# Kernel optimization log

Measured on AMD Instinct MI355X. Metric: run time of the kernel, lower is better.

## Reference

```python
import jax, jax.numpy as jnp
import numpy as np
from jax import lax


def conv2d_same(x, w):
    # x: [N,C,H,W], w: [O,I,3,3] -> [N,O,H,W], stride 1, padding 1
    return lax.conv_general_dilated(x, w, (1, 1), 'SAME',
                                    dimension_numbers=('NCHW', 'OIHW', 'NCHW'))


def bilinear_gather(x, py, px):
    # x: [N,C,H,W]; py,px: [N,K,H,W] float sampling coords (zero pad outside)
    # returns [N,C,K,H,W]
    N, C, H, W = x.shape
    y0f = jnp.floor(py)
    x0f = jnp.floor(px)
    wy = (py - y0f)[:, None]  # [N,1,K,H,W]
    wx = (px - x0f)[:, None]
    y0 = y0f.astype(jnp.int32)
    x0 = x0f.astype(jnp.int32)
    flat = x.reshape(N, C, H * W)

    def gather(yi, xi):
        valid = ((yi >= 0) & (yi < H) & (xi >= 0) & (xi < W))
        yc = jnp.clip(yi, 0, H - 1)
        xc = jnp.clip(xi, 0, W - 1)
        idx = (yc * W + xc).reshape(N, 1, -1)          # [N,1,K*H*W]
        g = jnp.take_along_axis(flat, jnp.broadcast_to(idx, (N, C, idx.shape[-1])), axis=2)
        g = g.reshape(N, C, *yi.shape[1:])             # [N,C,K,H,W]
        return g * valid.astype(x.dtype)[:, None]

    v00 = gather(y0, x0)
    v01 = gather(y0, x0 + 1)
    v10 = gather(y0 + 1, x0)
    v11 = gather(y0 + 1, x0 + 1)
    return (v00 * (1 - wy) * (1 - wx) + v01 * (1 - wy) * wx
            + v10 * wy * (1 - wx) + v11 * wy * wx)


def deform_conv(x, off, w, b):
    # x: [N,C,H,W]; off: [N,18,H,W] (dy,dx per 3x3 tap); w: [O,C,3,3]; b: [O]
    N, C, H, W = x.shape
    K = 9
    off = off.reshape(N, K, 2, H, W)
    kdy, kdx = jnp.meshgrid(jnp.arange(3) - 1, jnp.arange(3) - 1, indexing='ij')
    kdy = kdy.reshape(K).astype(x.dtype)
    kdx = kdx.reshape(K).astype(x.dtype)
    hh = jnp.arange(H, dtype=x.dtype)
    ww = jnp.arange(W, dtype=x.dtype)
    py = off[:, :, 0] + hh[None, None, :, None] + kdy[None, :, None, None]  # [N,K,H,W]
    px = off[:, :, 1] + ww[None, None, None, :] + kdx[None, :, None, None]
    sampled = bilinear_gather(x, py, px)               # [N,C,K,H,W]
    out = jnp.einsum('nckhw,ock->nohw', sampled, w.reshape(w.shape[0], C, K))
    return out + b[None, :, None, None]


def setup_inputs() -> dict:
    key = jax.random.key(0)
    ks = jax.random.split(key, 8)
    B, obj, C, H, W = 2, 4, 256, 48, 48
    return {
        'query': jax.random.normal(ks[0], (B, C, H, W), jnp.float32),
        'key': jax.random.normal(ks[1], (B, C, H, W), jnp.float32),
        'value': jax.random.normal(ks[2], (B, obj, C, H, W), jnp.float32),
        'off_conv_w': jax.random.normal(ks[3], (C, 2 * C, 3, 3), jnp.float32) * 0.02,
        'off_conv_b': jnp.zeros((C,), jnp.float32),
        'offp_w': jax.random.normal(ks[4], (18, C, 3, 3), jnp.float32) * 0.02,
        'offp_b': jnp.zeros((18,), jnp.float32),
        'deform_w': jax.random.normal(ks[5], (C, C, 3, 3), jnp.float32) * 0.02,
        'deform_b': jnp.zeros((C,), jnp.float32),
    }


def reference(query, key, value, off_conv_w, off_conv_b, offp_w, offp_b, deform_w, deform_b):
    B, obj, C, H, W = value.shape
    N = B * obj
    concat = jnp.concatenate([query, key], axis=1)                    # [B,2C,H,W]
    feat = conv2d_same(concat, off_conv_w) + off_conv_b[None, :, None, None]
    feat = jnp.broadcast_to(feat[:, None], (B, obj, C, H, W)).reshape(N, C, H, W)
    x = value.reshape(N, C, H, W)
    off = conv2d_same(feat, offp_w) + offp_b[None, :, None, None]     # [N,18,H,W]
    out = deform_conv(x, off, deform_w, deform_b)                     # [N,C,H,W]
    out = out.reshape(N, C, H * W).transpose(2, 0, 1)                 # [HW,N,C]
    q = jnp.broadcast_to(query[:, None], (B, obj, C, H, W)).reshape(N, C, H * W)
    return q.transpose(2, 0, 1) + out
```

## Files before the change

### kernel.cpp

```cpp
#include <hip/hip_runtime.h>

#define HH 48
#define WW 48
#define HWP 2304
#define CC 256
#define NB 8
#define QKROW 2305

typedef __attribute__((ext_vector_type(8))) short short8;
typedef __attribute__((ext_vector_type(4))) short bf16x4;
typedef __attribute__((ext_vector_type(4))) float floatx4;

static __device__ __forceinline__ unsigned short f2bf(float f) {
    union { float f; unsigned u; } v; v.f = f;
    unsigned r = v.u + 0x7fffu + ((v.u >> 16) & 1u);
    return (unsigned short)(r >> 16);
}
static __device__ __forceinline__ float bf2f(short v) {
    union { unsigned u; float f; } x; x.u = ((unsigned)(unsigned short)v) << 16;
    return x.f;
}

__global__ __launch_bounds__(256) void k_tr_qk(const float* __restrict__ q,
        const float* __restrict__ kk, unsigned short* __restrict__ qkT) {
    __shared__ float T[64][65];
    const int pg = blockIdx.x, cg = blockIdx.y;
    const int b = blockIdx.z >> 1, src = blockIdx.z & 1;
    const float* s = (src ? kk : q) + (size_t)b * CC * HWP;
    const int tx = threadIdx.x & 63, ty = threadIdx.x >> 6;
#pragma unroll
    for (int i = 0; i < 16; i++) {
        int cl = ty * 16 + i;
        T[cl][tx] = s[(size_t)(cg * 64 + cl) * HWP + pg * 64 + tx];
    }
    __syncthreads();
#pragma unroll
    for (int i = 0; i < 16; i++) {
        int pxl = ty * 16 + i;
        qkT[((size_t)b * QKROW + pg * 64 + pxl) * 512 + src * 256 + cg * 64 + tx]
            = f2bf(T[tx][pxl]);
    }
}

__global__ __launch_bounds__(256) void k_tr_v(const float* __restrict__ v,
                                              unsigned short* __restrict__ vT) {
    __shared__ float T[64][65];
    const int pg = blockIdx.x, cg = blockIdx.y, n = blockIdx.z;
    const float* s = v + (size_t)n * CC * HWP;
    const int tx = threadIdx.x & 63, ty = threadIdx.x >> 6;
#pragma unroll
    for (int i = 0; i < 16; i++) {
        int cl = ty * 16 + i;
        T[cl][tx] = s[(size_t)(cg * 64 + cl) * HWP + pg * 64 + tx];
    }
    __syncthreads();
#pragma unroll
    for (int i = 0; i < 16; i++) {
        int pxl = ty * 16 + i;
        vT[((size_t)n * HWP + pg * 64 + pxl) * 256 + cg * 64 + tx] = f2bf(T[tx][pxl]);
    }
}

__global__ __launch_bounds__(256) void k_prep_w(const float* __restrict__ w1,
        const float* __restrict__ dw, const float* __restrict__ w2,
        unsigned short* __restrict__ w1r, unsigned short* __restrict__ wdr,
        unsigned short* __restrict__ w2r, unsigned short* __restrict__ qkT,
        unsigned short* __restrict__ featb) {
    if (blockIdx.x == 7200) {
        int t = threadIdx.x;
#pragma unroll
        for (int b = 0; b < 2; b++) {
            qkT[((size_t)b * QKROW + HWP) * 512 + t] = 0;
            qkT[((size_t)b * QKROW + HWP) * 512 + 256 + t] = 0;
            featb[((size_t)b * QKROW + HWP) * 256 + t] = 0;
        }
        return;
    }
    int idx = blockIdx.x * 256 + threadIdx.x;
    if (idx < 1179648) {
        int j = idx & 7, l = (idx >> 3) & 63, mtg = (idx >> 9) & 15;
        int kk = (idx >> 13) & 15, tap = idx >> 17;
        int o = mtg * 16 + (l & 15);
        int c2 = kk * 32 + (l >> 4) * 8 + j;
        w1r[idx] = f2bf(w1[((size_t)o * 512 + c2) * 9 + tap]);
    } else if (idx < 1179648 + 589824) {
        int i2 = idx - 1179648;
        int j = i2 & 7, l = (i2 >> 3) & 63, mtg = (i2 >> 9) & 15;
        int kk = (i2 >> 13) & 7, tap = i2 >> 16;
        int o = mtg * 16 + (l & 15);
        int c = kk * 32 + (l >> 4) * 8 + j;
        wdr[i2] = f2bf(dw[((size_t)o * 256 + c) * 9 + tap]);
    } else {
        int i2 = idx - 1179648 - 589824;
        int j = i2 & 7, l = (i2 >> 3) & 63, mt = (i2 >> 9) & 1;
        int kk = (i2 >> 10) & 7, tap = i2 >> 13;
        int o = mt * 16 + (l & 15);
        int c = kk * 32 + (l >> 4) * 8 + j;
        w2r[i2] = (o < 18) ? f2bf(w2[((size_t)o * 256 + c) * 9 + tap]) : 0;
    }
}

__global__ __launch_bounds__(512, 4) void k_conv1(const unsigned short* __restrict__ qkT,
        const unsigned short* __restrict__ w1r, const float* __restrict__ b1,
        unsigned short* __restrict__ featb) {
    __shared__ __align__(16) unsigned short Bl[2][32 * 64 * 8];

    const int tid = threadIdx.x;
    const int pt = blockIdx.x;
    const int b  = blockIdx.y;
    const int oh = blockIdx.z;
    const int px0 = pt * 32;
    const int lane = tid & 63, wv = tid >> 6;
    const int lo = lane & 15, quad = lane >> 4;
    const int mtg = oh * 8 + wv;

    floatx4 acc[2];
    acc[0] = (floatx4)0.f; acc[1] = (floatx4)0.f;

    short8 R[4];
    auto stage_load = [&](int tap) {
        const int dy = tap / 3 - 1, dx = tap % 3 - 1;
#pragma unroll
        for (int k = 0; k < 4; k++) {
            int seg = tid + k * 512;
            int cl  = seg >> 6;
            int sl  = seg & 63;
            int px  = px0 + cl;
            int h = px / WW, w = px - (px / WW) * WW;
            bool val = (h + dy >= 0) && (h + dy < HH)
                       && (w + dx >= 0) && (w + dx < WW);
            int row = val ? (px + dy * WW + dx) : HWP;
            R[k] = *(const short8*)(qkT + ((size_t)b * QKROW + row) * 512 + sl * 8);
        }
    };

    stage_load(0);
    int buf = 0;

    for (int tap = 0; tap < 9; tap++) {
        unsigned short* sb = &Bl[buf][0];
#pragma unroll
        for (int k = 0; k < 4; k++) {
            int seg = tid + k * 512;
            int cl = seg >> 6, sl = seg & 63;
            int slw = sl ^ (cl & 7);
            *(short8*)(sb + ((size_t)cl * 64 + slw) * 8) = R[k];
        }
        __syncthreads();

        if (tap < 8) stage_load(tap + 1);

        const unsigned short* afr = w1r + (((size_t)tap * 16 * 16 + mtg) * 64 + lane) * 8;
#pragma unroll 4
        for (int ks = 0; ks < 16; ks++) {
            short8 a = *(const short8*)(afr + (size_t)ks * 16 * 512);
#pragma unroll
            for (int nt = 0; nt < 2; nt++) {
                int cl = nt * 16 + lo;
                int slot = (ks * 4 + quad) ^ (cl & 7);
                short8 bf = *(const short8*)(sb + ((size_t)cl * 64 + slot) * 8);
                acc[nt] = __builtin_amdgcn_mfma_f32_16x16x32_bf16(a, bf, acc[nt], 0, 0, 0);
            }
        }
        buf ^= 1;
    }

    const int o = mtg * 16 + quad * 4;
    const float b0 = b1[o], bb1 = b1[o + 1], bb2 = b1[o + 2], bb3 = b1[o + 3];
#pragma unroll
    for (int nt = 0; nt < 2; nt++) {
        int px = px0 + nt * 16 + lo;
        bf16x4 pk;
        pk[0] = (short)f2bf(acc[nt][0] + b0);
        pk[1] = (short)f2bf(acc[nt][1] + bb1);
        pk[2] = (short)f2bf(acc[nt][2] + bb2);
        pk[3] = (short)f2bf(acc[nt][3] + bb3);
        *(bf16x4*)(featb + ((size_t)b * QKROW + px) * 256 + o) = pk;
    }
}

__global__ __launch_bounds__(256) void k_conv2(const unsigned short* __restrict__ featb,
        const unsigned short* __restrict__ w2r, float* __restrict__ off9) {
    const int tid = threadIdx.x;
    const int pb = blockIdx.x;
    const int b  = blockIdx.y;
    const int tap = blockIdx.z;
    const int lane = tid & 63, wv = tid >> 6;
    const int lo = lane & 15, quad = lane >> 4;
    const int pp = pb * 64 + wv * 16 + lo;
    const int h = pp / WW, w = pp - (pp / WW) * WW;
    const int dy = tap / 3 - 1, dx = tap % 3 - 1;
    const bool val = (h + dy >= 0) && (h + dy < HH) && (w + dx >= 0) && (w + dx < WW);
    const int row = val ? (pp + dy * WW + dx) : HWP;

    const unsigned short* brow = featb + ((size_t)b * QKROW + row) * 256 + quad * 8;
    const unsigned short* afr = w2r + (((size_t)tap * 8 * 2) * 64 + lane) * 8;

    floatx4 acc[2];
    acc[0] = (floatx4)0.f; acc[1] = (floatx4)0.f;
#pragma unroll
    for (int ks = 0; ks < 8; ks++) {
        short8 bf = *(const short8*)(brow + ks * 32);
        const unsigned short* ak = afr + (size_t)ks * 2 * 512;
        short8 a0 = *(const short8*)(ak);
        short8 a1 = *(const short8*)(ak + 512);
        acc[0] = __builtin_amdgcn_mfma_f32_16x16x32_bf16(a0, bf, acc[0], 0, 0, 0);
        acc[1] = __builtin_amdgcn_mfma_f32_16x16x32_bf16(a1, bf, acc[1], 0, 0, 0);
    }

    float* dst = off9 + (((size_t)tap * 2 + b) * HWP + pp) * 32;
#pragma unroll
    for (int mt = 0; mt < 2; mt++) {
        int o = mt * 16 + quad * 4;
        *(floatx4*)(dst + o) = acc[mt];
    }
}

__global__ __launch_bounds__(256) void k_osum(const float* __restrict__ off9,
        const float* __restrict__ b2, float* __restrict__ off) {
    int i = blockIdx.x * 256 + threadIdx.x;
    int b = i / (18 * HWP);
    int r = i - b * 18 * HWP;
    int o = r / HWP, px = r - o * HWP;
    float s = b2[o];
#pragma unroll
    for (int t = 0; t < 9; t++)
        s += off9[(((size_t)t * 2 + b) * HWP + px) * 32 + o];
    off[i] = s;
}

__global__ __launch_bounds__(512, 2) void k_deform(const unsigned short* __restrict__ vT,
        const float* __restrict__ off, const unsigned short* __restrict__ wdr,
        const float* __restrict__ db, const float* __restrict__ q,
        float* __restrict__ out) {
    __shared__ __align__(16) unsigned short Sl[2][80 * 256];

    const int tid = threadIdx.x;
    const int bid = blockIdx.x;
    const int c0 = (((bid & 7) << 5) + (bid >> 3)) * 72;
    const int lane = tid & 63, wv = tid >> 6;
    const int lo = lane & 15, quad = lane >> 4;
    const int colg = tid >> 5;
    const int slice = tid & 31;

    int u_pq[5];
    float u_m[5];
    const float* u_off[5];
    const unsigned short* u_vT[5];
#pragma unroll
    for (int u = 0; u < 5; u++) {
        int cl = colg + u * 16;
        int cg = min(c0 + cl, 18431);
        int pq = cg >> 3, n = cg & 7;
        u_pq[u] = pq;
        u_m[u]  = (cl < 72) ? 1.f : 0.f;
        u_off[u] = off + (size_t)(n >> 2) * 18 * HWP + pq;
        u_vT[u]  = vT + (size_t)n * HWP * 256 + slice * 8;
    }

    floatx4 acc[2][5];
#pragma unroll
    for (int mt = 0; mt < 2; mt++)
#pragma unroll
        for (int nt = 0; nt < 5; nt++) acc[mt][nt] = (floatx4)0.f;

    short8 P[5][4];
    float  cwt[5][4];
    float  ndy[5], ndx[5];

    auto prefetch_off = [&](int tap) {
#pragma unroll
        for (int u = 0; u < 5; u++) {
            ndy[u] = u_off[u][(2 * tap) * HWP];
            ndx[u] = u_off[u][(2 * tap + 1) * HWP];
        }
    };

    auto prefetch_body = [&](int tap) {
        const float kdy = (float)(tap / 3 - 1), kdx = (float)(tap % 3 - 1);
#pragma unroll
        for (int u = 0; u < 5; u++) {
            int pq = u_pq[u];
            int h = pq / WW, w = pq - (pq / WW) * WW;
            float py = ndy[u] + (float)h + kdy;
            float px = ndx[u] + (float)w + kdx;
            float y0f = floorf(py), x0f = floorf(px);
            int y0 = (int)y0f, x0 = (int)x0f;
            float fy = py - y0f, fx = px - x0f;
            bool y0ok = (y0 >= 0) & (y0 < HH), y1ok = (y0 >= -1) & (y0 < HH - 1);
            bool x0ok = (x0 >= 0) & (x0 < WW), x1ok = (x0 >= -1) & (x0 < WW - 1);
            int y0c = min(max(y0, 0), HH - 1), y1c = min(max(y0 + 1, 0), HH - 1);
            int x0c = min(max(x0, 0), WW - 1), x1c = min(max(x0 + 1, 0), WW - 1);
            const unsigned short* r0 = u_vT[u] + (size_t)(y0c * WW + x0c) * 256;
            const unsigned short* r1 = u_vT[u] + (size_t)(y0c * WW + x1c) * 256;
            const unsigned short* r2 = u_vT[u] + (size_t)(y1c * WW + x0c) * 256;
            const unsigned short* r3 = u_vT[u] + (size_t)(y1c * WW + x1c) * 256;
            float m = u_m[u];
            cwt[u][0] = (y0ok && x0ok) ? m * (1.f - fy) * (1.f - fx) : 0.f;
            cwt[u][1] = (y0ok && x1ok) ? m * (1.f - fy) * fx         : 0.f;
            cwt[u][2] = (y1ok && x0ok) ? m * fy * (1.f - fx)         : 0.f;
            cwt[u][3] = (y1ok && x1ok) ? m * fy * fx                 : 0.f;
            P[u][0] = *(const short8*)(r0);
            P[u][1] = *(const short8*)(r1);
            P[u][2] = *(const short8*)(r2);
            P[u][3] = *(const short8*)(r3);
        }
    };

    prefetch_off(0);
    prefetch_body(0);
    int buf = 0;

    for (int tap = 0; tap < 9; tap++) {
        if (tap < 8) prefetch_off(tap + 1);
        unsigned short* sb = &Sl[buf][0];
#pragma unroll
        for (int u = 0; u < 5; u++) {
            float w0 = cwt[u][0], w1 = cwt[u][1], w2 = cwt[u][2], w3 = cwt[u][3];
            short8 ov;
#pragma unroll
            for (int j = 0; j < 8; j++) {
                float s = w0 * bf2f(P[u][0][j]) + w1 * bf2f(P[u][1][j])
                        + w2 * bf2f(P[u][2][j]) + w3 * bf2f(P[u][3][j]);
                ov[j] = (short)f2bf(s);
            }
            int cl = colg + u * 16;
            int slot = slice ^ (cl & 7);
            *(short8*)(sb + cl * 256 + slot * 8) = ov;
        }
        __syncthreads();

        if (tap < 8) prefetch_body(tap + 1);

        const unsigned short* afr = wdr + (((size_t)tap * 8 * 16 + wv * 2) * 64 + lane) * 8;
#pragma unroll
        for (int ks = 0; ks < 8; ks++) {
            const unsigned short* ak = afr + (size_t)ks * 16 * 512;
            short8 a0 = *(const short8*)(ak);
            short8 a1 = *(const short8*)(ak + 512);
#pragma unroll
            for (int nt = 0; nt < 5; nt++) {
                int cl = nt * 16 + lo;
                int slot = (ks * 4 + quad) ^ (cl & 7);
                short8 bf = *(const short8*)(sb + cl * 256 + slot * 8);
                acc[0][nt] = __builtin_amdgcn_mfma_f32_16x16x32_bf16(a0, bf, acc[0][nt], 0, 0, 0);
                acc[1][nt] = __builtin_amdgcn_mfma_f32_16x16x32_bf16(a1, bf, acc[1][nt], 0, 0, 0);
            }
        }
        __syncthreads();
        buf ^= 1;
    }

#pragma unroll
    for (int mt = 0; mt < 2; mt++) {
        int o = wv * 32 + mt * 16 + quad * 4;
        float d0 = db[o], d1 = db[o + 1], d2 = db[o + 2], d3 = db[o + 3];
#pragma unroll
        for (int nt = 0; nt < 5; nt++) {
            int cl = nt * 16 + lo;
            if (cl < 72) {
                int cg = c0 + cl;
                int pq = cg >> 3, b = (cg & 7) >> 2;
                floatx4 r = acc[mt][nt];
                r[0] += d0 + q[((size_t)b * CC + o + 0) * HWP + pq];
                r[1] += d1 + q[((size_t)b * CC + o + 1) * HWP + pq];
                r[2] += d2 + q[((size_t)b * CC + o + 2) * HWP + pq];
                r[3] += d3 + q[((size_t)b * CC + o + 3) * HWP + pq];
                *(floatx4*)(out + (size_t)cg * CC + o) = r;
            }
        }
    }
}

extern "C" void kernel_launch(void* const* d_in, const int* in_sizes, int n_in,
                              void* d_out, int out_size, void* d_ws, size_t ws_size,
                              hipStream_t stream) {
    const float* q  = (const float*)d_in[0];
    const float* k  = (const float*)d_in[1];
    const float* v  = (const float*)d_in[2];
    const float* w1 = (const float*)d_in[3];
    const float* b1 = (const float*)d_in[4];
    const float* w2 = (const float*)d_in[5];
    const float* b2 = (const float*)d_in[6];
    const float* dw = (const float*)d_in[7];
    const float* db = (const float*)d_in[8];
    float* out = (float*)d_out;

    float* off   = (float*)d_ws;
    float* feat3 = off + 82944;
    float* off9  = feat3 + 3538944;
    unsigned short* qkT   = (unsigned short*)(off9 + 1327104);
    unsigned short* vT    = qkT + 2360320;
    unsigned short* featb = vT + 4718592;
    unsigned short* w1r   = featb + 1180160;
    unsigned short* wdr   = w1r + 1179648;
    unsigned short* w2r   = wdr + 589824;

    hipLaunchKernelGGL(k_tr_qk, dim3(36, 4, 4),  dim3(256), 0, stream, q, k, qkT);
    hipLaunchKernelGGL(k_tr_v,  dim3(36, 4, 8),  dim3(256), 0, stream, v, vT);
    hipLaunchKernelGGL(k_prep_w,dim3(7201),      dim3(256), 0, stream, w1, dw, w2, w1r, wdr, w2r, qkT, featb);
    hipLaunchKernelGGL(k_conv1, dim3(72, 2, 2),  dim3(512), 0, stream, qkT, w1r, b1, featb);
    hipLaunchKernelGGL(k_conv2, dim3(36, 2, 9),  dim3(256), 0, stream, featb, w2r, off9);
    hipLaunchKernelGGL(k_osum,  dim3(324),       dim3(256), 0, stream, off9, b2, off);
    hipLaunchKernelGGL(k_deform,dim3(256),       dim3(512), 0, stream, vT, off, wdr, db, q, out);
}
```

Measured before the change: 208.5 us.

## Merge transpose kernels and add pixel-major query copy for deform epilogue

Folds the q/k and v transpose kernels into one launch indexed by blockIdx.z. While transposing the query, it also writes an fp32 pixel-major copy of it. The deform epilogue then reads the residual query as one contiguous float4 instead of four strided scalar loads spaced HWP apart. This costs an extra fp32 write of the query in the transpose pass and reuses the previously unused feat3 workspace region.

```diff
diff --git a/kernel.cpp b/kernel.cpp
--- a/kernel.cpp
+++ b/kernel.cpp
@@ -21,43 +21,45 @@
     return x.f;
 }
 
-__global__ __launch_bounds__(256) void k_tr_qk(const float* __restrict__ q,
-        const float* __restrict__ kk, unsigned short* __restrict__ qkT) {
+__global__ __launch_bounds__(256) void k_tr(const float* __restrict__ q,
+        const float* __restrict__ kk, const float* __restrict__ v,
+        unsigned short* __restrict__ qkT, float* __restrict__ qT,
+        unsigned short* __restrict__ vT) {
     __shared__ float T[64][65];
-    const int pg = blockIdx.x, cg = blockIdx.y;
-    const int b = blockIdx.z >> 1, src = blockIdx.z & 1;
-    const float* s = (src ? kk : q) + (size_t)b * CC * HWP;
+    const int pg = blockIdx.x, cg = blockIdx.y, z = blockIdx.z;
     const int tx = threadIdx.x & 63, ty = threadIdx.x >> 6;
-#pragma unroll
-    for (int i = 0; i < 16; i++) {
-        int cl = ty * 16 + i;
-        T[cl][tx] = s[(size_t)(cg * 64 + cl) * HWP + pg * 64 + tx];
-    }
-    __syncthreads();
-#pragma unroll
-    for (int i = 0; i < 16; i++) {
-        int pxl = ty * 16 + i;
-        qkT[((size_t)b * QKROW + pg * 64 + pxl) * 512 + src * 256 + cg * 64 + tx]
-            = f2bf(T[tx][pxl]);
-    }
-}
-
-__global__ __launch_bounds__(256) void k_tr_v(const float* __restrict__ v,
-                                              unsigned short* __restrict__ vT) {
-    __shared__ float T[64][65];
-    const int pg = blockIdx.x, cg = blockIdx.y, n = blockIdx.z;
-    const float* s = v + (size_t)n * CC * HWP;
-    const int tx = threadIdx.x & 63, ty = threadIdx.x >> 6;
-#pragma unroll
-    for (int i = 0; i < 16; i++) {
-        int cl = ty * 16 + i;
-        T[cl][tx] = s[(size_t)(cg * 64 + cl) * HWP + pg * 64 + tx];
-    }
-    __syncthreads();
-#pragma unroll
-    for (int i = 0; i < 16; i++) {
-        int pxl = ty * 16 + i;
-        vT[((size_t)n * HWP + pg * 64 + pxl) * 256 + cg * 64 + tx] = f2bf(T[tx][pxl]);
+    if (z < 4) {
+        const int b = z >> 1, src = z & 1;
+        const float* s = (src ? kk : q) + (size_t)b * CC * HWP;
+#pragma unroll
+        for (int i = 0; i < 16; i++) {
+            int cl = ty * 16 + i;
+            T[cl][tx] = s[(size_t)(cg * 64 + cl) * HWP + pg * 64 + tx];
+        }
+        __syncthreads();
+#pragma unroll
+        for (int i = 0; i < 16; i++) {
+            int pxl = ty * 16 + i;
+            float val = T[tx][pxl];
+            qkT[((size_t)b * QKROW + pg * 64 + pxl) * 512 + src * 256 + cg * 64 + tx]
+                = f2bf(val);
+            if (src == 0)
+                qT[((size_t)(pg * 64 + pxl) * 2 + b) * 256 + cg * 64 + tx] = val;
+        }
+    } else {
+        const int n = z - 4;
+        const float* s = v + (size_t)n * CC * HWP;
+#pragma unroll
+        for (int i = 0; i < 16; i++) {
+            int cl = ty * 16 + i;
+            T[cl][tx] = s[(size_t)(cg * 64 + cl) * HWP + pg * 64 + tx];
+        }
+        __syncthreads();
+#pragma unroll
+        for (int i = 0; i < 16; i++) {
+            int pxl = ty * 16 + i;
+            vT[((size_t)n * HWP + pg * 64 + pxl) * 256 + cg * 64 + tx] = f2bf(T[tx][pxl]);
+        }
     }
 }
 
@@ -231,7 +233,7 @@
 
 __global__ __launch_bounds__(512, 2) void k_deform(const unsigned short* __restrict__ vT,
         const float* __restrict__ off, const unsigned short* __restrict__ wdr,
-        const float* __restrict__ db, const float* __restrict__ q,
+        const float* __restrict__ db, const float* __restrict__ qT,
         float* __restrict__ out) {
     __shared__ __align__(16) unsigned short Sl[2][80 * 256];
 
@@ -361,11 +363,12 @@
             if (cl < 72) {
                 int cg = c0 + cl;
                 int pq = cg >> 3, b = (cg & 7) >> 2;
+                floatx4 qv = *(const floatx4*)(qT + ((size_t)pq * 2 + b) * 256 + o);
                 floatx4 r = acc[mt][nt];
-                r[0] += d0 + q[((size_t)b * CC + o + 0) * HWP + pq];
-                r[1] += d1 + q[((size_t)b * CC + o + 1) * HWP + pq];
-                r[2] += d2 + q[((size_t)b * CC + o + 2) * HWP + pq];
-                r[3] += d3 + q[((size_t)b * CC + o + 3) * HWP + pq];
+                r[0] += d0 + qv[0];
+                r[1] += d1 + qv[1];
+                r[2] += d2 + qv[2];
+                r[3] += d3 + qv[3];
                 *(floatx4*)(out + (size_t)cg * CC + o) = r;
             }
         }
@@ -387,8 +390,8 @@
     float* out = (float*)d_out;
 
     float* off   = (float*)d_ws;
-    float* feat3 = off + 82944;
-    float* off9  = feat3 + 3538944;
+    float* qT    = off + 82944;
+    float* off9  = qT + 3538944;
     unsigned short* qkT   = (unsigned short*)(off9 + 1327104);
     unsigned short* vT    = qkT + 2360320;
     unsigned short* featb = vT + 4718592;
@@ -396,11 +399,10 @@
     unsigned short* wdr   = w1r + 1179648;
     unsigned short* w2r   = wdr + 589824;
 
-    hipLaunchKernelGGL(k_tr_qk, dim3(36, 4, 4),  dim3(256), 0, stream, q, k, qkT);
-    hipLaunchKernelGGL(k_tr_v,  dim3(36, 4, 8),  dim3(256), 0, stream, v, vT);
+    hipLaunchKernelGGL(k_tr,    dim3(36, 4, 12), dim3(256), 0, stream, q, k, v, qkT, qT, vT);
     hipLaunchKernelGGL(k_prep_w,dim3(7201),      dim3(256), 0, stream, w1, dw, w2, w1r, wdr, w2r, qkT, featb);
     hipLaunchKernelGGL(k_conv1, dim3(72, 2, 2),  dim3(512), 0, stream, qkT, w1r, b1, featb);
     hipLaunchKernelGGL(k_conv2, dim3(36, 2, 9),  dim3(256), 0, stream, featb, w2r, off9);
     hipLaunchKernelGGL(k_osum,  dim3(324),       dim3(256), 0, stream, off9, b2, off);
-    hipLaunchKernelGGL(k_deform,dim3(256),       dim3(512), 0, stream, vT, off, wdr, db, q, out);
-}
+    hipLaunchKernelGGL(k_deform,dim3(256),       dim3(512), 0, stream, vT, off, wdr, db, qT, out);
+}
```

Result: no change. 207.3 us (-0.6%).
